# Kernel tuning notes

Hardware: AMD Instinct MI355X
Metric: run time of the kernel (lower is better)

The kernel has to match this reference:

```python
import jax, jax.numpy as jnp
import numpy as np

FACTOR = 1
EPS = 1e-8
SCALES = (1, 2, 4)


def _pool(x, scale):
    # adaptive_avg_pool1d along time with L % scale == 0 -> uniform bin mean
    if scale == 1:
        return x
    B, L, H, E = x.shape
    return x.reshape(B, L // scale, scale, H, E).mean(axis=2)


def _interp_linear(x, L_out):
    # F.interpolate(mode='linear', align_corners=False) along time axis (axis=1)
    B, Ls, H, E = x.shape
    i = jnp.arange(L_out, dtype=jnp.float32)
    src = jnp.maximum((i + 0.5) * (Ls / L_out) - 0.5, 0.0)
    x0 = jnp.floor(src).astype(jnp.int32)
    x1 = jnp.minimum(x0 + 1, Ls - 1)
    lam = (src - x0.astype(jnp.float32))[None, :, None, None]
    return x[:, x0] * (1.0 - lam) + x[:, x1] * lam


def _corr_agg(q, k, v, w1, b1, w2, b2, w3, b3):
    # q,k,v: [B, Ls, H, E]
    B, Ls, H, E = q.shape
    qf = jnp.fft.rfft(q.transpose(0, 2, 3, 1), axis=-1)   # [B,H,E,Lf]
    kf = jnp.fft.rfft(k.transpose(0, 2, 3, 1), axis=-1)
    corr = jnp.fft.irfft(qf * jnp.conj(kf), n=Ls, axis=-1).astype(jnp.float32)  # [B,H,E,Ls]

    # ---- adaptive-k features ----
    energy = jnp.mean(jnp.sum(corr ** 2, axis=(1, 2)))          # scalar, expanded to B
    var = jnp.var(corr.reshape(B, -1), axis=1, ddof=1)          # unbiased, like torch.var
    cm = corr.reshape(B, H * E, Ls).mean(axis=1)                # [B, Ls]
    pk = jnp.sum((cm[:, 1:-1] > cm[:, :-2]) & (cm[:, 1:-1] > cm[:, 2:]), axis=1).astype(jnp.float32)
    feats = jnp.stack([jnp.broadcast_to(energy, (B,)), var, pk], axis=1)  # [B,3]
    h = jax.nn.relu(feats @ w1.T + b1)
    h = jax.nn.relu(h @ w2.T + b2)
    ratio = jax.nn.sigmoid(h @ w3.T + b3)[:, 0]                 # [B]
    kvals = jnp.clip((ratio * Ls * FACTOR).astype(jnp.int32), 1, Ls)  # [B]

    # ---- adaptive time-delay aggregation ----
    c = corr.transpose(0, 3, 1, 2)                              # [B, Ls, H, E]
    interior = (c[:, 1:-1] > c[:, :-2]) & (c[:, 1:-1] > c[:, 2:])
    pad = jnp.zeros((B, 1, H, E), dtype=bool)
    peaks = jnp.concatenate([pad, interior, pad], axis=1)       # [B,Ls,H,E] local maxima

    neg_inf = jnp.float32(-jnp.inf)
    vals = jnp.where(peaks, c, neg_inf).reshape(B, -1)
    count = peaks.reshape(B, -1).sum(axis=1)
    sorted_desc = -jnp.sort(-vals, axis=1)
    thresh = jnp.take_along_axis(sorted_desc, (kvals - 1)[:, None], axis=1)[:, 0]  # k-th largest peak
    topk_mask = peaks & (c >= thresh[:, None, None, None])
    keep_topk = (count > kvals)[:, None, None, None]
    final = jnp.where(keep_topk, topk_mask, peaks)

    attn = jnp.where(final, c, 0.0)
    w = jax.nn.softmax(attn + EPS, axis=1)                      # softmax over time lags
    return w * v                                                # einsum('lhe,lhe->lhe') == elementwise


def setup_inputs() -> dict:
    key = jax.random.key(0)
    ks = jax.random.split(key, 10)
    B, L, H, E = 16, 1024, 8, 64
    return {
        "queries": jax.random.normal(ks[0], (B, L, H, E), jnp.float32),
        "keys": jax.random.normal(ks[1], (B, L, H, E), jnp.float32),
        "values": jax.random.normal(ks[2], (B, L, H, E), jnp.float32),
        "scale_weights": jax.random.normal(ks[3], (3,), jnp.float32) * 0.1 + 1.0 / 3.0,
        "k_w1": jax.random.normal(ks[4], (32, 3), jnp.float32) * 0.1,
        "k_b1": jax.random.normal(ks[5], (32,), jnp.float32) * 0.1,
        "k_w2": jax.random.normal(ks[6], (16, 32), jnp.float32) * 0.1,
        "k_b2": jax.random.normal(ks[7], (16,), jnp.float32) * 0.1,
        "k_w3": jax.random.normal(ks[8], (1, 16), jnp.float32) * 0.1,
        "k_b3": jax.random.normal(ks[9], (1,), jnp.float32) * 0.1,
    }


def reference(queries, keys, values, scale_weights, k_w1, k_b1, k_w2, k_b2, k_w3, k_b3):
    B, L, H, E = queries.shape
    out = jnp.zeros_like(queries)
    for i, scale in enumerate(SCALES):
        q, k, v = _pool(queries, scale), _pool(keys, scale), _pool(values, scale)
        o = _corr_agg(q, k, v, k_w1, k_b1, k_w2, k_b2, k_w3, k_b3)
        if scale > 1:
            o = _interp_linear(o, L)
        out = out + o * scale_weights[i]
    return out
```

## Files before the change

kernel.cpp:

```cpp
#include <hip/hip_runtime.h>
#include <math.h>

typedef unsigned int u32;
typedef unsigned long long u64;

#define B_ 16
#define L_ 1024
#define H_ 8
#define E_ 64
#define C_ 512
#define NB_SEL 8
#define GCH 8
#define TC 32
#define CAPR 160
#define CAP1 192

__device__ __forceinline__ size_t co(int sidx) {
  return sidx == 0 ? 0u : (sidx == 1 ? 8388608u : 12582912u);
}
__device__ __forceinline__ u32 pk_off(int sidx) {
  return sidx == 0 ? 0u : (sidx == 1 ? 3211264u : 4816896u);
}
__device__ __forceinline__ u32 pk_cap(int sidx) { return 200704u >> sidx; }

__device__ __forceinline__ u32 f2key(float f) {
  u32 u = __float_as_uint(f);
  return (u & 0x80000000u) ? ~u : (u | 0x80000000u);
}
__device__ __forceinline__ float key2f(u32 k) {
  u32 u = (k & 0x80000000u) ? (k ^ 0x80000000u) : ~k;
  return __uint_as_float(u);
}

using u32g = __attribute__((address_space(1))) const unsigned int;
using u32l = __attribute__((address_space(3))) unsigned int;
__device__ __forceinline__ void gload16(const float* g, float* l) {
  __builtin_amdgcn_global_load_lds((u32g*)g, (u32l*)l, 16, 0, 0);
}

__global__ void k_init(u32* histA, u32* histB, u32* peak_cnt, u32* done,
                       double* s1, double* s2, float* cm) {
  const int gid = blockIdx.x * 256 + threadIdx.x;
  const int gs = gridDim.x * 256;
  for (int i = gid; i < 3 * 16 * 256; i += gs) { histA[i] = 0; histB[i] = 0; }
  for (int i = gid; i < 3 * 16 * 1024; i += gs) cm[i] = 0.f;
  for (int i = gid; i < 3 * 16 * 16; i += gs) peak_cnt[i] = 0;
  for (int i = gid; i < 144; i += gs) done[i] = 0;
  for (int i = gid; i < 48; i += gs) { s1[i] = 0.0; s2[i] = 0.0; }
}

__launch_bounds__(512, 6)
__global__ void k_corr1(const float* __restrict__ Q, const float* __restrict__ K,
                        float* __restrict__ corr) {
  constexpr int LS = 1024;
  constexpr int LMASK = LS - 1;
  constexpr int NCHUNK = LS / TC;
  __shared__ float ks[CAP1 * 64];
  const int tid = threadIdx.x;
  const int e = tid & 63;
  const int slot16 = __builtin_amdgcn_readfirstlane((tid >> 6) << 4);
  const int wb = __builtin_amdgcn_readfirstlane((tid >> 6) << 8);
  const int bh = blockIdx.x;
  const int tau0 = blockIdx.y << 7;
  const int b = bh >> 3, h = bh & 7;
  const size_t gbase = (size_t)b * L_ * C_ + (size_t)h * 64;
  const int l16 = tid & 15;
  const int rbase = tid >> 4;
  const int bp0 = 112 - slot16;

  float acc[16];
#pragma unroll
  for (int i = 0; i < 16; ++i) acc[i] = 0.f;

  const float* qp = Q + gbase + e;

#pragma unroll
  for (int it = 0; it < 5; ++it) {
    int l = it * 32 + rbase;
    int tk = (l - tau0 - 127 + 2048) & LMASK;
    gload16(K + gbase + (size_t)tk * C_ + l16 * 4, ks + it * 2048 + wb);
  }
  __syncthreads();

  int cph = 0;
  for (int chunk = 0; chunk < NCHUNK; ++chunk) {
    const int t0 = chunk * TC;
    if (chunk + 1 < NCHUNK) {
      const int l0 = t0 + 160;
      int tk = (l0 + rbase - tau0 - 127 + 2048) & LMASK;
      int sp = cph + 160; if (sp >= CAP1) sp -= CAP1;
      gload16(K + gbase + (size_t)tk * C_ + l16 * 4, ks + sp * 64 + wb);
    }
    const float* qc = qp + (size_t)t0 * C_;
    int bp = bp0 + cph; if (bp >= CAP1) bp -= CAP1;
    float km[47];
    if (bp <= CAP1 - 31) {
#pragma unroll
      for (int m = 0; m < 31; ++m) km[m] = ks[(bp + m) * 64 + e];
    } else {
#pragma unroll
      for (int m = 0; m < 31; ++m) {
        int p = bp + m; if (p >= CAP1) p -= CAP1;
        km[m] = ks[p * 64 + e];
      }
    }
#pragma unroll
    for (int jt = 0; jt < 16; ++jt) {
      float qv = qc[(size_t)jt * C_];
#pragma unroll
      for (int i = 0; i < 16; ++i) acc[i] = fmaf(qv, km[15 + jt - i], acc[i]);
    }
    if (bp <= CAP1 - 47) {
#pragma unroll
      for (int m = 31; m < 47; ++m) km[m] = ks[(bp + m) * 64 + e];
    } else {
#pragma unroll
      for (int m = 31; m < 47; ++m) {
        int p = bp + m; if (p >= CAP1) p -= CAP1;
        km[m] = ks[p * 64 + e];
      }
    }
#pragma unroll
    for (int jt = 16; jt < 32; ++jt) {
      float qv = qc[(size_t)jt * C_];
#pragma unroll
      for (int i = 0; i < 16; ++i) acc[i] = fmaf(qv, km[15 + jt - i], acc[i]);
    }
    __syncthreads();
    cph += 32; if (cph >= CAP1) cph -= CAP1;
  }
  float* wt = ks;
#pragma unroll
  for (int i = 0; i < 16; ++i) wt[(slot16 + i) * 65 + e] = acc[i];
  __syncthreads();
  const int to = tid & 127;
  const size_t cbase = ((size_t)b * C_ + (size_t)h * 64) * LS + tau0 + to;
  for (int cr = tid >> 7; cr < 64; cr += 4)
    corr[cbase + (size_t)cr * LS] = wt[to * 65 + cr];
}

template<int S>
__device__ __forceinline__ float4 pool_load(const float* gp) {
  float4 v = *(const float4*)gp;
  if constexpr (S >= 2) {
    float4 v2 = *(const float4*)(gp + C_);
    v.x += v2.x; v.y += v2.y; v.z += v2.z; v.w += v2.w;
  }
  if constexpr (S == 4) {
    float4 v3 = *(const float4*)(gp + 2 * C_);
    float4 v4 = *(const float4*)(gp + 3 * C_);
    v.x += v3.x + v4.x; v.y += v3.y + v4.y;
    v.z += v3.z + v4.z; v.w += v3.w + v4.w;
  }
  constexpr float sc = (S == 1) ? 1.f : (S == 2) ? 0.5f : 0.25f;
  if constexpr (S >= 2) { v.x *= sc; v.y *= sc; v.z *= sc; v.w *= sc; }
  return v;
}

template<int S>
__launch_bounds__(256, 3)
__global__ void k_corr(const float* __restrict__ Q, const float* __restrict__ K,
                       float* __restrict__ corr) {
  constexpr int LS = 1024 / S;
  constexpr int LMASK = LS - 1;
  constexpr int NCHUNK = LS / TC;
  __shared__ float qs[TC * 64];
  __shared__ float ks[CAPR * 64];
  const int tid = threadIdx.x;
  const int e = tid & 63;
  const int slot32 = __builtin_amdgcn_readfirstlane((tid >> 6) << 5);
  const int bh = blockIdx.x;
  const int tau0 = blockIdx.y << 7;
  const int b = bh >> 3, h = bh & 7;
  const size_t gbase = (size_t)b * L_ * C_ + (size_t)h * 64;
  const int l16 = tid & 15;
  const int rbase = tid >> 4;
  const int bp0 = 96 - slot32;

  float acc[32];
#pragma unroll
  for (int i = 0; i < 32; ++i) acc[i] = 0.f;

  int cph = 0;
  for (int chunk = 0; chunk < NCHUNK; ++chunk) {
    const int t0 = chunk * TC;
    __syncthreads();
    {
#pragma unroll
      for (int it = 0; it < 2; ++it) {
        int row = rbase + it * 16;
        int traw = (t0 + row) * S;
        float4 v = pool_load<S>(Q + gbase + (size_t)traw * C_ + l16 * 4);
        *(float4*)(qs + row * 64 + l16 * 4) = v;
      }
      if (chunk == 0) {
#pragma unroll
        for (int it = 0; it < 10; ++it) {
          int l = rbase + it * 16;
          int tk = (l - tau0 - 127 + 2048) & LMASK;
          float4 v = pool_load<S>(K + gbase + (size_t)tk * S * C_ + l16 * 4);
          *(float4*)(ks + l * 64 + l16 * 4) = v;
        }
      } else {
        int sp = cph + 128; if (sp >= CAPR) sp -= CAPR;
#pragma unroll
        for (int it = 0; it < 2; ++it) {
          int row = rbase + it * 16;
          int l = t0 + 128 + row;
          int tk = (l - tau0 - 127 + 2048) & LMASK;
          int p = sp + row; if (p >= CAPR) p -= CAPR;
          float4 v = pool_load<S>(K + gbase + (size_t)tk * S * C_ + l16 * 4);
          *(float4*)(ks + p * 64 + l16 * 4) = v;
        }
      }
      __syncthreads();
    }
    int bp = bp0 + cph; if (bp >= CAPR) bp -= CAPR;
    float km[63];
    if (bp <= CAPR - 47) {
#pragma unroll
      for (int m = 0; m < 47; ++m) km[m] = ks[(bp + m) * 64 + e];
    } else {
#pragma unroll
      for (int m = 0; m < 47; ++m) {
        int p = bp + m; if (p >= CAPR) p -= CAPR;
        km[m] = ks[p * 64 + e];
      }
    }
#pragma unroll
    for (int jt = 0; jt < 16; ++jt) {
      float qv = qs[jt * 64 + e];
#pragma unroll
      for (int i = 0; i < 32; ++i) acc[i] = fmaf(qv, km[31 + jt - i], acc[i]);
    }
    if (bp <= CAPR - 63) {
#pragma unroll
      for (int m = 47; m < 63; ++m) km[m] = ks[(bp + m) * 64 + e];
    } else {
#pragma unroll
      for (int m = 47; m < 63; ++m) {
        int p = bp + m; if (p >= CAPR) p -= CAPR;
        km[m] = ks[p * 64 + e];
      }
    }
#pragma unroll
    for (int jt = 16; jt < 32; ++jt) {
      float qv = qs[jt * 64 + e];
#pragma unroll
      for (int i = 0; i < 32; ++i) acc[i] = fmaf(qv, km[31 + jt - i], acc[i]);
    }
    cph += 32; if (cph >= CAPR) cph -= CAPR;
  }
  __syncthreads();
  float* wt = ks;
#pragma unroll
  for (int i = 0; i < 32; ++i) wt[(slot32 + i) * 65 + e] = acc[i];
  __syncthreads();
  const int to = tid & 127;
  const size_t cbase = ((size_t)b * C_ + (size_t)h * 64) * LS + tau0 + to;
  for (int cr = tid >> 7; cr < 64; cr += 2)
    corr[cbase + (size_t)cr * LS] = wt[to * 65 + cr];
}

__launch_bounds__(256, 4)
__global__ void k_stats(const float* __restrict__ corrbase, float* __restrict__ cm,
                        double* s1, double* s2, u32* peak_cnt, u32* histA,
                        u32* pkbase) {
  __shared__ __align__(16) float rows[GCH * 1024];
  __shared__ u32 hist_s[256];
  __shared__ double red_d[8];
  __shared__ u32 wv[4], wbase[4];
  const int tid = threadIdx.x;
  const int sidx = blockIdx.z;
  const int b = blockIdx.y;
  const int sb = sidx * 16 + b;
  const int Ls = 1024 >> sidx;
  const int c0 = blockIdx.x * GCH;
  const int lane = tid & 63;
  const int wave = tid >> 6;
  hist_s[tid] = 0;
  {
    const float4* src4 =
        (const float4*)(corrbase + co(sidx) + ((size_t)b * C_ + c0) * Ls);
    float4* dst4 = (float4*)rows;
    const int n4 = GCH * Ls / 4;
    for (int i = tid; i < n4; i += 256) dst4[i] = src4[i];
  }
  __syncthreads();
  const int nt = Ls >> 8;
  float cmacc[4] = {0.f, 0.f, 0.f, 0.f};
  double ls1 = 0.0, ls2 = 0.0;
  u32 mycnt = 0;
  for (int g = 0; g < GCH; ++g) {
    const float* row = rows + g * Ls;
    for (int i = 0; i < nt; ++i) {
      int t = tid + (i << 8);
      float v = row[t];
      cmacc[i] += v;
      ls1 += (double)v;
      ls2 += (double)v * (double)v;
      bool pk = (t >= 1) && (t <= Ls - 2) && (v > row[t - 1]) && (v > row[t + 1]);
      if (pk) {
        ++mycnt;
        atomicAdd(&hist_s[f2key(v) >> 24], 1u);
      }
    }
  }
  u32 wc = mycnt;
  for (int off = 32; off; off >>= 1) wc += __shfl_down(wc, off, 64);
  if (lane == 0) wv[wave] = wc;
  __syncthreads();
  if (tid == 0) {
    u32 t = 0;
    for (int w = 0; w < 4; ++w) { wbase[w] = t; t += wv[w]; }
    u32 base = atomicAdd(&peak_cnt[sb * 16], t);
    for (int w = 0; w < 4; ++w) wbase[w] += base;
  }
  __syncthreads();
  const u32 cap = pk_cap(sidx);
  u32* dst_pk = pkbase + pk_off(sidx) + (u32)b * cap;
  u32 off_w = wbase[wave];
  const u64 below = (1ull << lane) - 1ull;
  for (int g = 0; g < GCH; ++g) {
    const float* row = rows + g * Ls;
    for (int i = 0; i < nt; ++i) {
      int t = tid + (i << 8);
      float v = row[t];
      bool pk = (t >= 1) && (t <= Ls - 2) && (v > row[t - 1]) && (v > row[t + 1]);
      u64 mask = __ballot(pk);
      if (pk) {
        u32 idx = off_w + (u32)__popcll(mask & below);
        if (idx < cap) dst_pk[idx] = f2key(v);
      }
      off_w += (u32)__popcll(mask);
    }
  }
  for (int i = 0; i < nt; ++i) {
    int t = tid + (i << 8);
    unsafeAtomicAdd(&cm[sb * 1024 + t], cmacc[i]);
  }
  for (int off = 32; off; off >>= 1) {
    ls1 += __shfl_down(ls1, off, 64);
    ls2 += __shfl_down(ls2, off, 64);
  }
  if (lane == 0) { red_d[wave] = ls1; red_d[4 + wave] = ls2; }
  __syncthreads();
  if (tid == 0) {
    unsafeAtomicAdd(&s1[sb], red_d[0] + red_d[1] + red_d[2] + red_d[3]);
    unsafeAtomicAdd(&s2[sb], red_d[4] + red_d[5] + red_d[6] + red_d[7]);
  }
  if (hist_s[tid]) atomicAdd(&histA[sb * 256 + tid], hist_s[tid]);
}

__global__ void k_mlp(const float* __restrict__ cm, const double* s1,
                      const double* s2, const u32* peak_cnt, const u32* histA,
                      int* rank_s, u32* prefix_s, u32* active, float* thresh,
                      const float* w1, const float* b1, const float* w2,
                      const float* b2, const float* w3, const float* b3) {
  __shared__ float wls[673];
  __shared__ float cmrow[1024];
  __shared__ int red_i[4];
  __shared__ u32 cum[256];
  const int tid = threadIdx.x;
  const int sb = blockIdx.x;
  const int sidx = sb >> 4;
  const int Ls = 1024 >> sidx;
  for (int i = tid; i < 96; i += 256) wls[i] = w1[i];
  for (int i = tid; i < 32; i += 256) wls[96 + i] = b1[i];
  for (int i = tid; i < 512; i += 256) wls[128 + i] = w2[i];
  if (tid < 16) wls[640 + tid] = b2[tid];
  if (tid < 16) wls[656 + tid] = w3[tid];
  if (tid == 0) wls[672] = b3[0];
  for (int i = tid; i < Ls; i += 256) cmrow[i] = cm[sb * 1024 + i];
  __syncthreads();
  int cnt = 0;
  for (int t = 1 + tid; t <= Ls - 2; t += 256) {
    float v = cmrow[t];
    cnt += (v > cmrow[t - 1]) && (v > cmrow[t + 1]);
  }
  for (int off = 32; off; off >>= 1) cnt += __shfl_down(cnt, off, 64);
  if ((tid & 63) == 0) red_i[tid >> 6] = cnt;
  __syncthreads();
  if (tid == 0) {
    double tot = 0.0;
    for (int j = 0; j < 16; ++j) tot += s2[sidx * 16 + j];
    float f0 = (float)(tot / (16.0 * (double)Ls));
    double N = (double)C_ * (double)Ls;
    float f1 = (float)((s2[sb] - s1[sb] * s1[sb] / N) / (N - 1.0));
    float f2 = (float)(red_i[0] + red_i[1] + red_i[2] + red_i[3]);
    float h1[32];
    for (int j = 0; j < 32; ++j)
      h1[j] = fmaxf(0.f, wls[j * 3] * f0 + wls[j * 3 + 1] * f1 + wls[j * 3 + 2] * f2 + wls[96 + j]);
    float h2[16];
    for (int j = 0; j < 16; ++j) {
      float a = wls[640 + j];
      for (int i = 0; i < 32; ++i) a += wls[128 + j * 32 + i] * h1[i];
      h2[j] = fmaxf(0.f, a);
    }
    float z = wls[672];
    for (int i = 0; i < 16; ++i) z += wls[656 + i] * h2[i];
    float ratio = 1.0f / (1.0f + __expf(-z));
    int kv = (int)(ratio * (float)Ls);
    kv = min(max(kv, 1), Ls);
    int cntb = (int)peak_cnt[sb * 16];
    active[sb] = (u32)(cntb > kv);
    thresh[sb] = -INFINITY;
    rank_s[sb] = kv;
    prefix_s[sb] = 0;
  }
  __syncthreads();
  cum[tid] = histA[sb * 256 + tid];
  __syncthreads();
  for (int off = 1; off < 256; off <<= 1) {
    u32 add = (tid + off < 256) ? cum[tid + off] : 0u;
    __syncthreads();
    cum[tid] += add;
    __syncthreads();
  }
  u32 act_b = active[sb];
  u32 r = act_b ? (u32)rank_s[sb] : 0u;
  u32 cc = cum[tid];
  u32 cnext = (tid == 255) ? 0u : cum[tid + 1];
  __syncthreads();
  if (act_b && r > 0 && cc >= r && cnext < r) {
    prefix_s[sb] = (u32)tid << 24;
    rank_s[sb] = (int)(r - cnext);
  }
}

__global__ void k_sel(const u32* __restrict__ pkbase, const u32* peak_cnt,
                      const u32* active, int* rank_s, u32* prefix_s,
                      u32* hist, u32* done, float* thresh, int level) {
  __shared__ u32 hist_s[256];
  __shared__ u32 cum[256];
  __shared__ u32 islast;
  const int tid = threadIdx.x;
  const int sb = blockIdx.x / NB_SEL;
  const int blk = blockIdx.x % NB_SEL;
  const int sidx = sb >> 4;
  hist_s[tid] = 0;
  if (tid == 0) islast = 0;
  __syncthreads();
  const int act = (int)active[sb];
  const u32 cap = pk_cap(sidx);
  u32 cnt = peak_cnt[sb * 16];
  if (cnt > cap) cnt = cap;
  if (act) {
    const u32 pref = prefix_s[sb];
    const int hi_sh = 32 - 8 * level;
    const int b_sh = 24 - 8 * level;
    const u32 lo = (u32)(((u64)cnt * (u64)blk) / NB_SEL);
    const u32 hi = (u32)(((u64)cnt * (u64)(blk + 1)) / NB_SEL);
    const u32* src = pkbase + pk_off(sidx) + (u32)(sb & 15) * cap;
    for (u32 i = lo + tid; i < hi; i += 256) {
      u32 key = src[i];
      if ((key >> hi_sh) == (pref >> hi_sh))
        atomicAdd(&hist_s[(key >> b_sh) & 255u], 1u);
    }
  }
  __syncthreads();
  if (hist_s[tid]) atomicAdd(&hist[sb * 256 + tid], hist_s[tid]);
  __syncthreads();
  if (tid == 0) {
    __threadfence();
    u32 t = atomicAdd(&done[(level - 1) * 48 + sb], 1u);
    if (t == NB_SEL - 1) islast = 1;
  }
  __syncthreads();
  if (!islast) return;
  __threadfence();
  u32 hv = atomicAdd(&hist[sb * 256 + tid], 0u);
  cum[tid] = hv;
  hist[sb * 256 + tid] = 0;
  __syncthreads();
  for (int off = 1; off < 256; off <<= 1) {
    u32 add = (tid + off < 256) ? cum[tid + off] : 0u;
    __syncthreads();
    cum[tid] += add;
    __syncthreads();
  }
  u32 r = act ? (u32)rank_s[sb] : 0u;
  u32 pref2 = act ? prefix_s[sb] : 0u;
  u32 cc = cum[tid];
  u32 cnext = (tid == 255) ? 0u : cum[tid + 1];
  __syncthreads();
  if (act && r > 0 && cc >= r && cnext < r) {
    u32 np = pref2 | ((u32)tid << (24 - 8 * level));
    prefix_s[sb] = np;
    rank_s[sb] = (int)(r - cnext);
    if (level == 3) thresh[sb] = key2f(np);
  }
}

__global__ void k_softstats(const float* __restrict__ corrbase, const float* thresh,
                            float2* __restrict__ mZ) {
  __shared__ float row[1024];
  __shared__ float red_s[8];
  const int tid = threadIdx.x;
  const int bc = blockIdx.x;
  const int sidx = blockIdx.y;
  const int Ls = 1024 >> sidx;
  const float th = thresh[sidx * 16 + (bc >> 9)];
  const float* src = corrbase + co(sidx) + (size_t)bc * Ls;
  for (int t = tid; t < Ls; t += 256) row[t] = src[t];
  __syncthreads();
  float mx = 0.f;
  for (int t = tid; t < Ls; t += 256) {
    float v = row[t];
    bool pk = (t >= 1) && (t <= Ls - 2) && (v > row[t - 1]) && (v > row[t + 1]) && (v >= th);
    if (pk) mx = fmaxf(mx, v);
  }
  for (int off = 32; off; off >>= 1) mx = fmaxf(mx, __shfl_down(mx, off, 64));
  if ((tid & 63) == 0) red_s[tid >> 6] = mx;
  __syncthreads();
  float m = fmaxf(fmaxf(red_s[0], red_s[1]), fmaxf(red_s[2], red_s[3]));
  float zs = 0.f;
  for (int t = tid; t < Ls; t += 256) {
    float v = row[t];
    bool pk = (t >= 1) && (t <= Ls - 2) && (v > row[t - 1]) && (v > row[t + 1]) && (v >= th);
    float a = pk ? v : 0.f;
    zs += __expf(a - m);
  }
  for (int off = 32; off; off >>= 1) zs += __shfl_down(zs, off, 64);
  if ((tid & 63) == 0) red_s[4 + (tid >> 6)] = zs;
  __syncthreads();
  if (tid == 0) {
    float Z = red_s[4] + red_s[5] + red_s[6] + red_s[7];
    mZ[sidx * 8192 + bc] = make_float2(m, 1.0f / Z);
  }
}

__launch_bounds__(256, 4)
__global__ void k_apply(const float* __restrict__ corr, const float* __restrict__ V,
                        const float2* __restrict__ mZ, const float* thresh,
                        float* __restrict__ o, int Ls, int s) {
  __shared__ float ct[64][131];
  __shared__ float m_s[64], rz_s[64];
  const int tid = threadIdx.x;
  const int b = blockIdx.z;
  const int c0 = blockIdx.y << 6;
  const int t0 = blockIdx.x << 7;
  {
    const int row0 = tid >> 7, jc = tid & 127;
    for (int rr = row0; rr < 64; rr += 2) {
      const float* src = corr + ((size_t)b * C_ + c0 + rr) * Ls;
      for (int j = jc; j < 130; j += 128) {
        int t = t0 - 1 + j;
        t = max(0, min(t, Ls - 1));
        ct[rr][j] = src[t];
      }
    }
  }
  if (tid < 64) {
    float2 v = mZ[b * C_ + c0 + tid];
    m_s[tid] = v.x; rz_s[tid] = v.y;
  }
  __syncthreads();
  const float th = thresh[b];
  const int cl = tid & 63, ts = tid >> 6;
  for (int ii = 0; ii < 32; ++ii) {
    int tl = ts + (ii << 2);
    int tg = t0 + tl;
    float vm = ct[cl][tl], vc = ct[cl][tl + 1], vp = ct[cl][tl + 2];
    bool pk = (tg >= 1) && (tg <= Ls - 2) && (vc > vm) && (vc > vp) && (vc >= th);
    float a = pk ? vc : 0.f;
    float w = __expf(a - m_s[cl]) * rz_s[cl];
    size_t vb = ((size_t)b * L_ + (size_t)tg * s) * C_ + c0 + cl;
    float vv;
    if (s == 2) vv = (V[vb] + V[vb + C_]) * 0.5f;
    else vv = ((V[vb] + V[vb + C_]) + (V[vb + 2 * C_] + V[vb + 3 * C_])) * 0.25f;
    o[((size_t)b * Ls + tg) * C_ + c0 + cl] = w * vv;
  }
}

__launch_bounds__(256, 4)
__global__ void k_apply_final(const float* __restrict__ corr, const float* __restrict__ V,
                              const float2* __restrict__ mZ, const float* thresh,
                              const float* __restrict__ o2, const float* __restrict__ o4,
                              const float* __restrict__ sw, float* __restrict__ out) {
  __shared__ float ct[64][131];
  __shared__ float m_s[64], rz_s[64];
  const int Ls = 1024;
  const int tid = threadIdx.x;
  const int b = blockIdx.z;
  const int c0 = blockIdx.y << 6;
  const int t0 = blockIdx.x << 7;
  {
    const int row0 = tid >> 7, jc = tid & 127;
    for (int rr = row0; rr < 64; rr += 2) {
      const float* src = corr + ((size_t)b * C_ + c0 + rr) * Ls;
      for (int j = jc; j < 130; j += 128) {
        int t = t0 - 1 + j;
        t = max(0, min(t, Ls - 1));
        ct[rr][j] = src[t];
      }
    }
  }
  if (tid < 64) {
    float2 v = mZ[b * C_ + c0 + tid];
    m_s[tid] = v.x; rz_s[tid] = v.y;
  }
  __syncthreads();
  const float th = thresh[b];
  const float sw0 = sw[0], sw1 = sw[1], sw2 = sw[2];
  const int cl = tid & 63, ts = tid >> 6;
  for (int ii = 0; ii < 32; ++ii) {
    int tl = ts + (ii << 2);
    int tg = t0 + tl;
    float vm = ct[cl][tl], vc = ct[cl][tl + 1], vp = ct[cl][tl + 2];
    bool pk = (tg >= 1) && (tg <= Ls - 2) && (vc > vm) && (vc > vp) && (vc >= th);
    float a = pk ? vc : 0.f;
    float w = __expf(a - m_s[cl]) * rz_s[cl];
    float v1 = V[((size_t)b * L_ + tg) * C_ + c0 + cl];
    float r = sw0 * w * v1;
    {
      float srcp = fmaxf((tg + 0.5f) * 0.5f - 0.5f, 0.f);
      int x0 = (int)srcp;
      float lam = srcp - (float)x0;
      int x1 = min(x0 + 1, 511);
      const float* p = o2 + (size_t)b * 512 * C_ + c0 + cl;
      r += sw1 * ((1.f - lam) * p[(size_t)x0 * C_] + lam * p[(size_t)x1 * C_]);
    }
    {
      float srcp = fmaxf((tg + 0.5f) * 0.25f - 0.5f, 0.f);
      int x0 = (int)srcp;
      float lam = srcp - (float)x0;
      int x1 = min(x0 + 1, 255);
      const float* p = o4 + (size_t)b * 256 * C_ + c0 + cl;
      r += sw2 * ((1.f - lam) * p[(size_t)x0 * C_] + lam * p[(size_t)x1 * C_]);
    }
    out[((size_t)b * L_ + tg) * C_ + c0 + cl] = r;
  }
}

extern "C" void kernel_launch(void* const* d_in, const int* in_sizes, int n_in,
                              void* d_out, int out_size, void* d_ws, size_t ws_size,
                              hipStream_t stream) {
  const float* Q  = (const float*)d_in[0];
  const float* Kk = (const float*)d_in[1];
  const float* V  = (const float*)d_in[2];
  const float* sw = (const float*)d_in[3];
  const float* w1 = (const float*)d_in[4];
  const float* b1 = (const float*)d_in[5];
  const float* w2 = (const float*)d_in[6];
  const float* b2 = (const float*)d_in[7];
  const float* w3 = (const float*)d_in[8];
  const float* b3 = (const float*)d_in[9];
  float* out = (float*)d_out;

  char* ws = (char*)d_ws;
  size_t p = 0;
  auto alloc = [&](size_t n) { char* r = ws + p; p = (p + n + 255) & ~(size_t)255; return r; };
  float*  corr = (float*)alloc((size_t)(8388608 + 4194304 + 2097152) * 4);
  char*   oreg = alloc((size_t)25165824);
  float*  o2   = (float*)oreg;
  float*  o4   = (float*)(oreg + 16777216);
  u32*    pk   = (u32*)oreg;
  float*  cm       = (float*)alloc(3 * 16 * 1024 * 4);
  float2* mZ       = (float2*)alloc(3 * 16 * 512 * 8);
  double* s1d      = (double*)alloc(48 * 8);
  double* s2d      = (double*)alloc(48 * 8);
  u32*    histA    = (u32*)alloc(3 * 16 * 256 * 4);
  u32*    histB    = (u32*)alloc(3 * 16 * 256 * 4);
  u32*    peak_cnt = (u32*)alloc(3 * 16 * 16 * 4);
  u32*    done     = (u32*)alloc(144 * 4);
  int*    rank_s   = (int*)alloc(48 * 4);
  u32*    prefix_s = (u32*)alloc(48 * 4);
  u32*    active   = (u32*)alloc(48 * 4);
  float*  thresh   = (float*)alloc(48 * 4);

  k_init<<<dim3(16), dim3(256), 0, stream>>>(histA, histB, peak_cnt, done,
                                             s1d, s2d, cm);
  k_corr1<<<dim3(128, 8), dim3(512), 0, stream>>>(Q, Kk, corr);
  k_corr<2><<<dim3(128, 4), dim3(256), 0, stream>>>(Q, Kk, corr + 8388608);
  k_corr<4><<<dim3(128, 2), dim3(256), 0, stream>>>(Q, Kk, corr + 12582912);
  k_stats<<<dim3(C_ / GCH, B_, 3), dim3(256), 0, stream>>>(
      corr, cm, s1d, s2d, peak_cnt, histA, pk);
  k_mlp<<<dim3(48), dim3(256), 0, stream>>>(
      cm, s1d, s2d, peak_cnt, histA, rank_s, prefix_s, active, thresh,
      w1, b1, w2, b2, w3, b3);
  for (int level = 1; level <= 3; ++level)
    k_sel<<<dim3(48 * NB_SEL), dim3(256), 0, stream>>>(
        pk, peak_cnt, active, rank_s, prefix_s, histB, done, thresh, level);
  k_softstats<<<dim3(8192, 3), dim3(256), 0, stream>>>(corr, thresh, mZ);
  k_apply<<<dim3(2, 8, 16), dim3(256), 0, stream>>>(
      corr + 12582912, V, mZ + 2 * 8192, thresh + 32, o4, 256, 4);
  k_apply<<<dim3(4, 8, 16), dim3(256), 0, stream>>>(
      corr + 8388608, V, mZ + 1 * 8192, thresh + 16, o2, 512, 2);
  k_apply_final<<<dim3(8, 8, 16), dim3(256), 0, stream>>>(
      corr, V, mZ, thresh, o2, o4, sw, out);
}
```

Measured before the change: 928.0 us.

## Transpose K ring in LDS with XOR swizzle and stage Q via double-buffered LDS

The correlation kernel now keeps K in a transposed, XOR-swizzled LDS layout (one row per channel, with a mirrored tail that removes ring-wrap branches). This lets each thread read its 47-tap K window as twelve vector loads instead of scalar ones. Q is staged through a double-buffered LDS tile with vector reads in place of per-tap global loads. Register prefetch of the next chunk replaces the async global-to-LDS copies, and occupancy drops from 6 to 4 blocks because LDS use and register pressure both grow.

```diff
diff --git a/kernel.cpp b/kernel.cpp
--- a/kernel.cpp
+++ b/kernel.cpp
@@ -3,6 +3,7 @@
 
 typedef unsigned int u32;
 typedef unsigned long long u64;
+typedef float f4 __attribute__((ext_vector_type(4)));
 
 #define B_ 16
 #define L_ 1024
@@ -14,6 +15,8 @@
 #define TC 32
 #define CAPR 160
 #define CAP1 192
+#define KW 256
+#define QW 32
 
 __device__ __forceinline__ size_t co(int sidx) {
   return sidx == 0 ? 0u : (sidx == 1 ? 8388608u : 12582912u);
@@ -30,12 +33,6 @@
 __device__ __forceinline__ float key2f(u32 k) {
   u32 u = (k & 0x80000000u) ? (k ^ 0x80000000u) : ~k;
   return __uint_as_float(u);
-}
-
-using u32g = __attribute__((address_space(1))) const unsigned int;
-using u32l = __attribute__((address_space(3))) unsigned int;
-__device__ __forceinline__ void gload16(const float* g, float* l) {
-  __builtin_amdgcn_global_load_lds((u32g*)g, (u32l*)l, 16, 0, 0);
 }
 
 __global__ void k_init(u32* histA, u32* histB, u32* peak_cnt, u32* done,
@@ -49,87 +46,101 @@
   for (int i = gid; i < 48; i += gs) { s1[i] = 0.0; s2[i] = 0.0; }
 }
 
-__launch_bounds__(512, 6)
+__launch_bounds__(512, 4)
 __global__ void k_corr1(const float* __restrict__ Q, const float* __restrict__ K,
                         float* __restrict__ corr) {
   constexpr int LS = 1024;
   constexpr int LMASK = LS - 1;
   constexpr int NCHUNK = LS / TC;
-  __shared__ float ks[CAP1 * 64];
+  __shared__ __align__(16) float ksT[64 * KW];
+  __shared__ __align__(16) float qT[2 * 64 * QW];
   const int tid = threadIdx.x;
   const int e = tid & 63;
-  const int slot16 = __builtin_amdgcn_readfirstlane((tid >> 6) << 4);
-  const int wb = __builtin_amdgcn_readfirstlane((tid >> 6) << 8);
+  const int w = tid >> 6;
+  const int slot16 = __builtin_amdgcn_readfirstlane(w << 4);
   const int bh = blockIdx.x;
   const int tau0 = blockIdx.y << 7;
   const int b = bh >> 3, h = bh & 7;
   const size_t gbase = (size_t)b * L_ * C_ + (size_t)h * 64;
-  const int l16 = tid & 15;
-  const int rbase = tid >> 4;
+  const int x4 = (e & 7) << 2;
   const int bp0 = 112 - slot16;
+  float* krow = ksT + e * KW;
+  float* qrow0 = qT + e * QW;
+  float* qrow1 = qT + 2048 + e * QW;
 
   float acc[16];
 #pragma unroll
   for (int i = 0; i < 16; ++i) acc[i] = 0.f;
 
-  const float* qp = Q + gbase + e;
-
-#pragma unroll
-  for (int it = 0; it < 5; ++it) {
-    int l = it * 32 + rbase;
-    int tk = (l - tau0 - 127 + 2048) & LMASK;
-    gload16(K + gbase + (size_t)tk * C_ + l16 * 4, ks + it * 2048 + wb);
+#pragma unroll
+  for (int pass = 0; pass < 5; ++pass) {
+    const int p0 = pass * 32 + (w << 2);
+    f4 v;
+#pragma unroll
+    for (int j = 0; j < 4; ++j) {
+      int tk = (p0 + j - tau0 - 127 + 2048) & LMASK;
+      v[j] = K[gbase + (size_t)tk * C_ + e];
+    }
+    *(f4*)&krow[p0 ^ x4] = v;
+    if (p0 < 47) *(f4*)&krow[(p0 + 192) ^ x4] = v;
+  }
+  {
+    f4 v;
+#pragma unroll
+    for (int j = 0; j < 4; ++j)
+      v[j] = Q[gbase + (size_t)((w << 2) + j) * C_ + e];
+    *(f4*)&qrow0[(w << 2) ^ x4] = v;
   }
   __syncthreads();
 
   int cph = 0;
   for (int chunk = 0; chunk < NCHUNK; ++chunk) {
     const int t0 = chunk * TC;
-    if (chunk + 1 < NCHUNK) {
-      const int l0 = t0 + 160;
-      int tk = (l0 + rbase - tau0 - 127 + 2048) & LMASK;
+    const bool more = (chunk + 1 < NCHUNK);
+    f4 kr, qr;
+    int spw = 0;
+    if (more) {
       int sp = cph + 160; if (sp >= CAP1) sp -= CAP1;
-      gload16(K + gbase + (size_t)tk * C_ + l16 * 4, ks + sp * 64 + wb);
-    }
-    const float* qc = qp + (size_t)t0 * C_;
+      spw = sp + (w << 2);
+#pragma unroll
+      for (int j = 0; j < 4; ++j) {
+        int l = t0 + 160 + (w << 2) + j;
+        int tk = (l - tau0 - 127 + 2048) & LMASK;
+        kr[j] = K[gbase + (size_t)tk * C_ + e];
+      }
+#pragma unroll
+      for (int j = 0; j < 4; ++j)
+        qr[j] = Q[gbase + (size_t)(t0 + TC + (w << 2) + j) * C_ + e];
+    }
     int bp = bp0 + cph; if (bp >= CAP1) bp -= CAP1;
-    float km[47];
-    if (bp <= CAP1 - 31) {
-#pragma unroll
-      for (int m = 0; m < 31; ++m) km[m] = ks[(bp + m) * 64 + e];
-    } else {
-#pragma unroll
-      for (int m = 0; m < 31; ++m) {
-        int p = bp + m; if (p >= CAP1) p -= CAP1;
-        km[m] = ks[p * 64 + e];
-      }
-    }
-#pragma unroll
-    for (int jt = 0; jt < 16; ++jt) {
-      float qv = qc[(size_t)jt * C_];
-#pragma unroll
-      for (int i = 0; i < 16; ++i) acc[i] = fmaf(qv, km[15 + jt - i], acc[i]);
-    }
-    if (bp <= CAP1 - 47) {
-#pragma unroll
-      for (int m = 31; m < 47; ++m) km[m] = ks[(bp + m) * 64 + e];
-    } else {
-#pragma unroll
-      for (int m = 31; m < 47; ++m) {
-        int p = bp + m; if (p >= CAP1) p -= CAP1;
-        km[m] = ks[p * 64 + e];
-      }
-    }
-#pragma unroll
-    for (int jt = 16; jt < 32; ++jt) {
-      float qv = qc[(size_t)jt * C_];
-#pragma unroll
-      for (int i = 0; i < 16; ++i) acc[i] = fmaf(qv, km[15 + jt - i], acc[i]);
+    f4 km4[12];
+#pragma unroll
+    for (int j = 0; j < 12; ++j)
+      km4[j] = *(const f4*)&krow[(bp + 4 * j) ^ x4];
+    const float* qb = (chunk & 1) ? qrow1 : qrow0;
+#pragma unroll
+    for (int g = 0; g < 8; ++g) {
+      f4 qv = *(const f4*)&qb[(g << 2) ^ x4];
+#pragma unroll
+      for (int k = 0; k < 4; ++k) {
+        const int jt = (g << 2) + k;
+#pragma unroll
+        for (int i = 0; i < 16; ++i) {
+          const int m = 15 + jt - i;
+          acc[i] = fmaf(qv[k], km4[m >> 2][m & 3], acc[i]);
+        }
+      }
+    }
+    if (more) {
+      *(f4*)&krow[spw ^ x4] = kr;
+      if (spw < 47) *(f4*)&krow[(spw + 192) ^ x4] = kr;
+      float* qn = (chunk & 1) ? qrow0 : qrow1;
+      *(f4*)&qn[(w << 2) ^ x4] = qr;
     }
     __syncthreads();
     cph += 32; if (cph >= CAP1) cph -= CAP1;
   }
-  float* wt = ks;
+  float* wt = ksT;
 #pragma unroll
   for (int i = 0; i < 16; ++i) wt[(slot16 + i) * 65 + e] = acc[i];
   __syncthreads();
```

Result: faster. 808.1 us (-12.9%).
